# Kernel optimization log

Measured on AMD Instinct MI355X. Metric: run time of the kernel, lower is better.

The kernel has to match this reference:

```python
import jax, jax.numpy as jnp
import numpy as np

# Sizes (must match input_specs)
N_CHR, E_CHR = 50000, 500000
N_SLV, E_SLV = 30000, 300000
B = 256            # number of graphs in the batch
FEAT = 64          # num_node_feats
DIM = 128          # hidden dim
HALF = DIM // 2    # last GCN layer output
ENS = 3            # ensemble per branch type


def setup_inputs() -> dict:
    key = jax.random.key(0)
    ks = jax.random.split(key, 20)
    g = lambda k, shape, fan_in: jax.random.normal(k, shape, dtype=jnp.float32) / np.sqrt(fan_in)
    inp = {
        'chr_x': jax.random.normal(ks[0], (N_CHR, FEAT), dtype=jnp.float32),
        'slv_x': jax.random.normal(ks[1], (N_SLV, FEAT), dtype=jnp.float32),
        'chr_edge_index': jax.random.randint(ks[2], (2, E_CHR), 0, N_CHR),
        'slv_edge_index': jax.random.randint(ks[3], (2, E_SLV), 0, N_SLV),
        'chr_x_batch': jnp.sort(jax.random.randint(ks[4], (N_CHR,), 0, B)),
        'slv_x_batch': jnp.sort(jax.random.randint(ks[5], (N_SLV,), 0, B)),
        # GCN weights, stacked over ensemble (GCNConv: bias=False)
        'chr_W0': g(ks[6], (ENS, FEAT, DIM), FEAT),
        'chr_W1': g(ks[7], (ENS, DIM, DIM), DIM),
        'chr_W2': g(ks[8], (ENS, DIM, HALF), DIM),
        'slv_W0': g(ks[9], (ENS, FEAT, DIM), FEAT),
        'slv_W1': g(ks[10], (ENS, DIM, DIM), DIM),
        'slv_W2': g(ks[11], (ENS, DIM, HALF), DIM),
        # per-ensemble projection heads (nn.Linear with bias)
        'cfc_W': g(ks[12], (ENS, HALF, DIM), HALF),
        'cfc_b': jnp.zeros((ENS, DIM), dtype=jnp.float32),
        'sfc_W': g(ks[13], (ENS, HALF, DIM), HALF),
        'sfc_b': jnp.zeros((ENS, DIM), dtype=jnp.float32),
        # final MLP head
        'fc1_W': g(ks[14], (2 * ENS * DIM, DIM), 2 * ENS * DIM),
        'fc1_b': jnp.zeros((DIM,), dtype=jnp.float32),
        'fc2_W': g(ks[15], (DIM, 1), DIM),
        'fc2_b': jnp.zeros((1,), dtype=jnp.float32),
    }
    return inp


def _gcn(x, W, src, dst, n_nodes):
    # GCNConv(normalize=False, bias=False, aggr='add'):
    # out[i] = sum_{(j,i) in E} (x @ W)[j]   (no self-loops, no normalization)
    h = x @ W
    return jax.ops.segment_sum(h[src], dst, num_segments=n_nodes)


def _branch(x, W0, W1, W2, edge_index, batch_ids, n_nodes):
    src, dst = edge_index[0], edge_index[1]
    h = jax.nn.relu(_gcn(x, W0, src, dst, n_nodes))
    h = jax.nn.relu(_gcn(h, W1, src, dst, n_nodes))
    h = jax.nn.relu(_gcn(h, W2, src, dst, n_nodes))
    # global_add_pool
    return jax.ops.segment_sum(h, batch_ids, num_segments=B)  # [B, HALF]


def reference(chr_x, slv_x, chr_W0, chr_W1, chr_W2, slv_W0, slv_W1, slv_W2,
              cfc_W, cfc_b, sfc_W, sfc_b, fc1_W, fc1_b, fc2_W, fc2_b,
              chr_edge_index, slv_edge_index, chr_x_batch, slv_x_batch):
    # vmap over the ensemble dimension (independent GCN stacks share inputs)
    rep_chr = jax.vmap(lambda w0, w1, w2: _branch(chr_x, w0, w1, w2, chr_edge_index, chr_x_batch, N_CHR))(
        chr_W0, chr_W1, chr_W2)  # [ENS, B, HALF]
    rep_slv = jax.vmap(lambda w0, w1, w2: _branch(slv_x, w0, w1, w2, slv_edge_index, slv_x_batch, N_SLV))(
        slv_W0, slv_W1, slv_W2)  # [ENS, B, HALF]
    ind_chr = jax.nn.relu(jnp.einsum('ebd,edh->ebh', rep_chr, cfc_W) + cfc_b[:, None, :])  # [ENS, B, DIM]
    ind_slv = jax.nn.relu(jnp.einsum('ebd,edh->ebh', rep_slv, sfc_W) + sfc_b[:, None, :])
    # torch.cat(ind_chr + ind_slv, dim=1): chr branches first, then slv branches
    hg = jnp.concatenate([
        jnp.transpose(ind_chr, (1, 0, 2)).reshape(B, ENS * DIM),
        jnp.transpose(ind_slv, (1, 0, 2)).reshape(B, ENS * DIM)], axis=1)  # [B, 2*ENS*DIM]
    hg = jax.nn.relu(hg @ fc1_W + fc1_b)
    out = hg @ fc2_W + fc2_b  # [B, 1]
    return out
```

## Files before the change

kernel.cpp:

```cpp
#include <hip/hip_runtime.h>

#define N_CHR 50000
#define E_CHR 500000
#define N_SLV 30000
#define E_SLV 300000
#define E_TOT (E_CHR + E_SLV)
#define BATCH_B 256
#define FEAT 64
#define DIM 128
#define HALF 64
#define ENSN 3
#define CB_CHR ((N_CHR + 255) / 256)
#define CB_SLV ((N_SLV + 255) / 256)
#define CB_TOT (CB_CHR + CB_SLV)
#define NBLK 128
#define CHUNK ((E_TOT + NBLK - 1) / NBLK)

typedef unsigned int u32;
typedef unsigned short u16;
typedef __attribute__((ext_vector_type(8))) short short8;
typedef __attribute__((ext_vector_type(4))) float floatx4;
typedef __attribute__((ext_vector_type(4))) unsigned int u32x4;


__device__ inline u16 f2b(float f) {
    u32 u = __builtin_bit_cast(u32, f);
    u += 0x7FFFu + ((u >> 16) & 1u);
    return (u16)(u >> 16);
}
__device__ inline float b2f_lo(u32 v) { return __builtin_bit_cast(float, v << 16); }
__device__ inline float b2f_hi(u32 v) { return __builtin_bit_cast(float, v & 0xFFFF0000u); }
__device__ inline u32 packb(float a, float b) { return (u32)f2b(a) | ((u32)f2b(b) << 16); }

__device__ inline void acc8(float* a, u32x4 v) {
    a[0] += b2f_lo(v.x); a[1] += b2f_hi(v.x);
    a[2] += b2f_lo(v.y); a[3] += b2f_hi(v.y);
    a[4] += b2f_lo(v.z); a[5] += b2f_hi(v.z);
    a[6] += b2f_lo(v.w); a[7] += b2f_hi(v.w);
}


__global__ void xconv_k(const float* __restrict__ xc, const float* __restrict__ xs,
                        u16* __restrict__ oc, u16* __restrict__ os) {
    const int nc = N_CHR * FEAT, ns = N_SLV * FEAT;
    int i = blockIdx.x * blockDim.x + threadIdx.x;
    int stride = gridDim.x * blockDim.x;
    for (; i < nc + ns; i += stride) {
        if (i < nc) oc[i] = f2b(xc[i]);
        else os[i - nc] = f2b(xs[i - nc]);
    }
}


__global__ void wconv6_k(const float* __restrict__ cW0, const float* __restrict__ cW1,
                         const float* __restrict__ cW2, const float* __restrict__ sW0,
                         const float* __restrict__ sW1, const float* __restrict__ sW2,
                         u16* __restrict__ cW0t, u16* __restrict__ cW1t, u16* __restrict__ cW2t,
                         u16* __restrict__ sW0t, u16* __restrict__ sW1t, u16* __restrict__ sW2t) {
    int z = blockIdx.z, e = blockIdx.y;
    const float* W; u16* Wt; int K, N;
    switch (z) {
        case 0: W = cW0; Wt = cW0t; K = FEAT; N = DIM;  break;
        case 1: W = cW1; Wt = cW1t; K = DIM;  N = DIM;  break;
        case 2: W = cW2; Wt = cW2t; K = DIM;  N = HALF; break;
        case 3: W = sW0; Wt = sW0t; K = FEAT; N = DIM;  break;
        case 4: W = sW1; Wt = sW1t; K = DIM;  N = DIM;  break;
        default: W = sW2; Wt = sW2t; K = DIM; N = HALF; break;
    }
    int idx = blockIdx.x * 256 + threadIdx.x;
    if (idx >= K * N) return;
    int k = idx / N, nn = idx - k * N;
    Wt[((size_t)e * N + nn) * K + k] = f2b(W[(size_t)e * K * N + idx]);
}


__global__ __launch_bounds__(256) void hist_blocks_k(
        const int* __restrict__ cdst, const int* __restrict__ sdst,
        int* __restrict__ gh, int* __restrict__ btot) {
    __shared__ int h[CB_TOT];
    int blk = blockIdx.x, t = threadIdx.x;
    for (int i = t; i < CB_TOT; i += 256) h[i] = 0;
    __syncthreads();
    int s = blk * CHUNK, e = s + CHUNK;
    if (e > E_TOT) e = E_TOT;
    for (int i = s + t; i < e; i += 256) {
        int bkt = (i < E_CHR) ? (cdst[i] >> 8) : (CB_CHR + (sdst[i - E_CHR] >> 8));
        atomicAdd(&h[bkt], 1);
    }
    __syncthreads();
    for (int j = t; j < CB_TOT; j += 256) {
        gh[j * NBLK + blk] = h[j];
        if (h[j]) atomicAdd(&btot[j], h[j]);
    }
}

__global__ void coarse_scan_k(const int* __restrict__ cnt, int* __restrict__ off) {
    int t = threadIdx.x;
    const int PER = (CB_TOT + 63) / 64;
    int loc[PER];
    int sum = 0;
    int s = t * PER;
#pragma unroll
    for (int k = 0; k < PER; k++) {
        int i = s + k;
        int v = (i < CB_TOT) ? cnt[i] : 0;
        loc[k] = sum;
        sum += v;
    }
    int inc = sum;
#pragma unroll
    for (int o = 1; o < 64; o <<= 1) {
        int sh = __shfl_up(inc, o, 64);
        if (t >= o) inc += sh;
    }
    int pre = inc - sum;
#pragma unroll
    for (int k = 0; k < PER; k++) {
        int i = s + k;
        if (i < CB_TOT) off[i] = pre + loc[k];
    }
    if (t == 63) off[CB_TOT] = inc;
}

__global__ __launch_bounds__(NBLK) void block_base_k(int* __restrict__ gh,
                                                     const int* __restrict__ coff) {
    int j = blockIdx.x, t = threadIdx.x;
    int v = gh[j * NBLK + t];
    int lane = t & 63, wv = t >> 6;
    int inc = v;
#pragma unroll
    for (int o = 1; o < 64; o <<= 1) {
        int sh = __shfl_up(inc, o, 64);
        if (lane >= o) inc += sh;
    }
    __shared__ int ws[2];
    if (lane == 63) ws[wv] = inc;
    __syncthreads();
    int p = inc - v + (wv ? ws[0] : 0);
    gh[j * NBLK + t] = coff[j] + p;
}

__global__ __launch_bounds__(256) void scatter2_k(
        const int* __restrict__ cei, const int* __restrict__ sei,
        const int* __restrict__ gh, u32* __restrict__ staging) {
    __shared__ int cur[CB_TOT];
    int blk = blockIdx.x, t = threadIdx.x;
    for (int j = t; j < CB_TOT; j += 256) cur[j] = gh[j * NBLK + blk];
    __syncthreads();
    int s = blk * CHUNK, e = s + CHUNK;
    if (e > E_TOT) e = E_TOT;
    for (int i = s + t; i < e; i += 256) {
        int src, dst, bkt;
        if (i < E_CHR) {
            src = cei[i]; dst = cei[E_CHR + i]; bkt = dst >> 8;
        } else {
            int j2 = i - E_CHR;
            src = sei[j2]; dst = sei[E_SLV + j2]; bkt = CB_CHR + (dst >> 8);
        }
        int p = atomicAdd(&cur[bkt], 1);
        staging[p] = (u32)src | ((u32)(dst & 255) << 17);
    }
}

__device__ inline int block_exscan(int v) {
    int lane = threadIdx.x & 63, wv = threadIdx.x >> 6;
    int inc = v;
#pragma unroll
    for (int o = 1; o < 64; o <<= 1) {
        int t = __shfl_up(inc, o, 64);
        if (lane >= o) inc += t;
    }
    __shared__ int ws[4];
    if (lane == 63) ws[wv] = inc;
    __syncthreads();
    if (threadIdx.x == 0) {
        int c = 0;
#pragma unroll
        for (int k = 0; k < 4; k++) { int t = ws[k]; ws[k] = c; c += t; }
    }
    __syncthreads();
    int r = ws[wv] + inc - v;
    __syncthreads();
    return r;
}

__global__ __launch_bounds__(256) void bucket_sort_k(
        const u32* __restrict__ staging, const int* __restrict__ coff,
        int* __restrict__ off_c, int* __restrict__ off_s,
        int* __restrict__ csr_c, int* __restrict__ csr_s) {
    int b = blockIdx.x, t = threadIdx.x;
    int isS = b >= CB_CHR;
    int base = coff[b], end = coff[b + 1];
    int n = isS ? N_SLV : N_CHR;
    int* off = isS ? off_s : off_c;
    int* csr = isS ? csr_s : csr_c;
    int outBase = isS ? base - E_CHR : base;
    int nodeBase = (isS ? (b - CB_CHR) : b) << 8;
    __shared__ int hist[256];
    __shared__ int cur[256];
    hist[t] = 0;
    __syncthreads();
    for (int i = base + t; i < end; i += 256)
        atomicAdd(&hist[staging[i] >> 17], 1);
    __syncthreads();
    int p = block_exscan(hist[t]);
    int node = nodeBase + t;
    if (node <= n) off[node] = outBase + p;
    cur[t] = p;
    __syncthreads();
    for (int i = base + t; i < end; i += 256) {
        u32 v = staging[i];
        int pos = atomicAdd(&cur[v >> 17], 1);
        csr[outBase + pos] = (int)(v & 0x1FFFFu);
    }
}


__global__ __launch_bounds__(256) void agg1_k(
        const u16* __restrict__ Xc, const int* __restrict__ offc, const int* __restrict__ csrc,
        u16* __restrict__ Yc, int nc,
        const u16* __restrict__ Xs, const int* __restrict__ offs, const int* __restrict__ csrs,
        u16* __restrict__ Ys, int ns) {
    int z = blockIdx.z;
    const u32x4* X4 = (const u32x4*)(z ? Xs : Xc);
    const int* off = z ? offs : offc;
    const int* csr = z ? csrs : csrc;
    u32x4* Y4 = (u32x4*)(z ? Ys : Yc);
    int n = z ? ns : nc;
    int i = blockIdx.x * 32 + (threadIdx.x >> 3);
    if (i >= n) return;
    int l8 = threadIdx.x & 7;
    int s = off[i], e2 = off[i + 1];
    float a[8] = {0.f, 0.f, 0.f, 0.f, 0.f, 0.f, 0.f, 0.f};
    int j = s;
    for (; j + 1 < e2; j += 2) {
        u32x4 v0 = X4[(size_t)csr[j] * 8 + l8];
        u32x4 v1 = X4[(size_t)csr[j + 1] * 8 + l8];
        acc8(a, v0); acc8(a, v1);
    }
    if (j < e2) acc8(a, X4[(size_t)csr[j] * 8 + l8]);
    u32x4 o;
    o.x = packb(a[0], a[1]); o.y = packb(a[2], a[3]);
    o.z = packb(a[4], a[5]); o.w = packb(a[6], a[7]);
    Y4[(size_t)i * 8 + l8] = o;
}


__global__ __launch_bounds__(256) void aggb128_k(
        const u16* __restrict__ Hc, const int* __restrict__ offc, const int* __restrict__ csrc,
        u16* __restrict__ Yc, int nc,
        const u16* __restrict__ Hs, const int* __restrict__ offs, const int* __restrict__ csrs,
        u16* __restrict__ Ys, int ns) {
    int z = blockIdx.z, e = blockIdx.y;
    int n = z ? ns : nc;
    const int* off = z ? offs : offc;
    const int* csr = z ? csrs : csrc;
    const u32x4* He = (const u32x4*)((z ? Hs : Hc) + (size_t)e * n * DIM);
    u32x4* Ye = (u32x4*)((z ? Ys : Yc) + (size_t)e * n * DIM);
    int i = blockIdx.x * 16 + (threadIdx.x >> 4);
    if (i >= n) return;
    int l16 = threadIdx.x & 15;
    int s = off[i], e2 = off[i + 1];
    float a[8] = {0.f, 0.f, 0.f, 0.f, 0.f, 0.f, 0.f, 0.f};
    int j = s;
    for (; j + 1 < e2; j += 2) {
        u32x4 v0 = He[(size_t)csr[j] * 16 + l16];
        u32x4 v1 = He[(size_t)csr[j + 1] * 16 + l16];
        acc8(a, v0); acc8(a, v1);
    }
    if (j < e2) acc8(a, He[(size_t)csr[j] * 16 + l16]);
    u32x4 o;
    o.x = packb(a[0], a[1]); o.y = packb(a[2], a[3]);
    o.z = packb(a[4], a[5]); o.w = packb(a[6], a[7]);
    Ye[(size_t)i * 16 + l16] = o;
}


#define WPAD 8

template<int K, int COLS, bool RELU>
__global__ __launch_bounds__(256) void gemm_mfma_k(
        const u16* __restrict__ Xc, size_t esc, const u16* __restrict__ Wtc,
        u16* __restrict__ Yc, int nc,
        const u16* __restrict__ Xs, size_t ess, const u16* __restrict__ Wts,
        u16* __restrict__ Ys, int ns) {
    __shared__ u16 wlds[COLS * (K + WPAD)];
    const int z = blockIdx.z, e = blockIdx.y;
    const int n = z ? ns : nc;
    const u16* Xe = (z ? Xs : Xc) + (size_t)e * (z ? ess : esc);
    const u16* We = (z ? Wts : Wtc) + (size_t)e * COLS * K;
    u16* Ye = (z ? Ys : Yc) + (size_t)e * (size_t)n * COLS;
    for (int c = threadIdx.x; c < COLS * (K / 8); c += 256) {
        int row = c / (K / 8), seg = c - row * (K / 8);
        *(short8*)(wlds + row * (K + WPAD) + seg * 8) = *(const short8*)(We + (size_t)row * K + seg * 8);
    }
    __syncthreads();
    int wave = threadIdx.x >> 6, lane = threadIdx.x & 63;
    int quad = lane >> 4, nq = lane & 15;
    int m0 = blockIdx.x * 256 + wave * 64;
    if (m0 >= n) return;
    constexpr int NT = COLS / 16, KT = K / 32;
    floatx4 acc[4][NT];
#pragma unroll
    for (int rg = 0; rg < 4; rg++)
#pragma unroll
        for (int t = 0; t < NT; t++) acc[rg][t] = (floatx4)(0.f);
#pragma unroll
    for (int kt = 0; kt < KT; kt++) {
        int k0 = kt * 32 + quad * 8;
        short8 a[4];
#pragma unroll
        for (int rg = 0; rg < 4; rg++) {
            int row = m0 + rg * 16 + nq;
            int rc = row < n ? row : n - 1;
            a[rg] = *(const short8*)(Xe + (size_t)rc * K + k0);
        }
#pragma unroll
        for (int t = 0; t < NT; t++) {
            short8 b = *(const short8*)(wlds + (t * 16 + nq) * (K + WPAD) + k0);
#pragma unroll
            for (int rg = 0; rg < 4; rg++)
                acc[rg][t] = __builtin_amdgcn_mfma_f32_16x16x32_bf16(a[rg], b, acc[rg][t], 0, 0, 0);
        }
    }
    int rbase = quad * 4;
#pragma unroll
    for (int rg = 0; rg < 4; rg++)
#pragma unroll
        for (int t = 0; t < NT; t++)
#pragma unroll
            for (int r = 0; r < 4; r++) {
                int row = m0 + rg * 16 + rbase + r;
                if (row < n) {
                    float v = acc[rg][t][r];
                    if (RELU) v = fmaxf(v, 0.f);
                    Ye[(size_t)row * COLS + t * 16 + nq] = f2b(v);
                }
            }
}


__global__ __launch_bounds__(256) void gemm23_k(
        const u16* __restrict__ Xc, const u16* __restrict__ W1c, const u16* __restrict__ W2c,
        u16* __restrict__ Yc, int nc,
        const u16* __restrict__ Xs, const u16* __restrict__ W1s, const u16* __restrict__ W2s,
        u16* __restrict__ Ys, int ns) {
    __shared__ u16 wlds[DIM * DIM];
    __shared__ u16 hlds[4 * 32 * DIM];
    const int z = blockIdx.z, e = blockIdx.y;
    const int n = z ? ns : nc;
    const u16* Xe = (z ? Xs : Xc) + (size_t)e * (size_t)n * DIM;
    const u16* W1 = (z ? W1s : W1c) + (size_t)e * DIM * DIM;
    const u16* W2 = (z ? W2s : W2c) + (size_t)e * HALF * DIM;
    u16* Ye = (z ? Ys : Yc) + (size_t)e * (size_t)n * HALF;
    for (int c = threadIdx.x; c < DIM * (DIM / 8); c += 256) {
        int row = c >> 4, seg = c & 15;
        *(short8*)(wlds + row * DIM + ((seg ^ (row & 15)) << 3)) =
            *(const short8*)(W1 + (size_t)row * DIM + (seg << 3));
    }
    __syncthreads();
    int wave = threadIdx.x >> 6, lane = threadIdx.x & 63;
    int quad = lane >> 4, nq = lane & 15;
    int m0 = blockIdx.x * 128 + wave * 32;
    floatx4 acc[2][8];
#pragma unroll
    for (int rg = 0; rg < 2; rg++)
#pragma unroll
        for (int t = 0; t < 8; t++) acc[rg][t] = (floatx4)(0.f);
#pragma unroll
    for (int kt = 0; kt < 4; kt++) {
        int k0 = kt * 32 + quad * 8;
        short8 a[2];
#pragma unroll
        for (int rg = 0; rg < 2; rg++) {
            int row = m0 + rg * 16 + nq;
            int rc = row < n ? row : (n - 1);
            a[rg] = *(const short8*)(Xe + (size_t)rc * DIM + k0);
        }
#pragma unroll
        for (int t = 0; t < 8; t++) {
            int rb = t * 16 + nq;
            short8 b = *(const short8*)(wlds + rb * DIM + ((((kt << 2) + quad) ^ nq) << 3));
#pragma unroll
            for (int rg = 0; rg < 2; rg++)
                acc[rg][t] = __builtin_amdgcn_mfma_f32_16x16x32_bf16(a[rg], b, acc[rg][t], 0, 0, 0);
        }
    }
    u16* hw = hlds + wave * 32 * DIM;
#pragma unroll
    for (int rg = 0; rg < 2; rg++)
#pragma unroll
        for (int t = 0; t < 8; t++)
#pragma unroll
            for (int r = 0; r < 4; r++) {
                int rl = rg * 16 + quad * 4 + r;
                int col = t * 16 + nq;
                hw[rl * DIM + (((col >> 3) ^ (rl & 15)) << 3) + (col & 7)] =
                    f2b(fmaxf(acc[rg][t][r], 0.f));
            }
    __syncthreads();
    for (int c = threadIdx.x; c < HALF * (DIM / 8); c += 256) {
        int row = c >> 4, seg = c & 15;
        *(short8*)(wlds + row * DIM + ((seg ^ (row & 15)) << 3)) =
            *(const short8*)(W2 + (size_t)row * DIM + (seg << 3));
    }
    __syncthreads();
    floatx4 acc2[2][4];
#pragma unroll
    for (int rg = 0; rg < 2; rg++)
#pragma unroll
        for (int t = 0; t < 4; t++) acc2[rg][t] = (floatx4)(0.f);
#pragma unroll
    for (int kt = 0; kt < 4; kt++) {
        int k0q = (kt << 2) + quad;
        short8 a[2];
#pragma unroll
        for (int rg = 0; rg < 2; rg++) {
            int rl = rg * 16 + nq;
            a[rg] = *(const short8*)(hw + rl * DIM + ((k0q ^ (rl & 15)) << 3));
        }
#pragma unroll
        for (int t = 0; t < 4; t++) {
            int rb = t * 16 + nq;
            short8 b = *(const short8*)(wlds + rb * DIM + ((k0q ^ nq) << 3));
#pragma unroll
            for (int rg = 0; rg < 2; rg++)
                acc2[rg][t] = __builtin_amdgcn_mfma_f32_16x16x32_bf16(a[rg], b, acc2[rg][t], 0, 0, 0);
        }
    }
#pragma unroll
    for (int rg = 0; rg < 2; rg++)
#pragma unroll
        for (int t = 0; t < 4; t++)
#pragma unroll
            for (int r = 0; r < 4; r++) {
                int row = m0 + rg * 16 + quad * 4 + r;
                if (row < n) Ye[(size_t)row * HALF + t * 16 + nq] = f2b(acc2[rg][t][r]);
            }
}


__global__ __launch_bounds__(256) void agg64pool_k(
        const u16* __restrict__ Pc, const int* __restrict__ offc, const int* __restrict__ csrc,
        const int* __restrict__ batc, int nc,
        const u16* __restrict__ Ps, const int* __restrict__ offs, const int* __restrict__ csrs,
        const int* __restrict__ bats, int ns,
        float* __restrict__ rep) {
    int z = blockIdx.z, e = blockIdx.y;
    int n = z ? ns : nc;
    const int* off = z ? offs : offc;
    const int* csr = z ? csrs : csrc;
    const int* batch = z ? bats : batc;
    const u32x4* He = (const u32x4*)((z ? Ps : Pc) + (size_t)e * n * HALF);
    int i0 = blockIdx.x * 32;
    int nl = threadIdx.x >> 3, l8 = threadIdx.x & 7;
    int i = i0 + nl;
    float a[8] = {0.f, 0.f, 0.f, 0.f, 0.f, 0.f, 0.f, 0.f};
    if (i < n) {
        int s = off[i], e2 = off[i + 1];
        int j = s;
        for (; j + 1 < e2; j += 2) {
            u32x4 v0 = He[(size_t)csr[j] * 8 + l8];
            u32x4 v1 = He[(size_t)csr[j + 1] * 8 + l8];
            acc8(a, v0); acc8(a, v1);
        }
        if (j < e2) acc8(a, He[(size_t)csr[j] * 8 + l8]);
    }
    __shared__ float sm[32][64];
    __shared__ int gb[32];
#pragma unroll
    for (int k = 0; k < 8; k++) sm[nl][l8 * 8 + k] = fmaxf(a[k], 0.f);
    if (threadIdx.x < 32) gb[threadIdx.x] = (i0 + (int)threadIdx.x < n) ? batch[i0 + threadIdx.x] : -1;
    __syncthreads();
    if (threadIdx.x < 64) {
        int f = threadIdx.x;
        int colbase = z * (ENSN * HALF) + e * HALF + f;
        float acc = 0.f;
        int g = -2;
        for (int k = 0; k < 32; k++) {
            int gg = gb[k];
            if (gg != g) {
                if (g >= 0) atomicAdd(&rep[g * (2 * ENSN * HALF) + colbase], acc);
                acc = 0.f;
                g = gg;
            }
            if (gg >= 0) acc += sm[k][f];
        }
        if (g >= 0) atomicAdd(&rep[g * (2 * ENSN * HALF) + colbase], acc);
    }
}


__global__ __launch_bounds__(256) void headfinal_k(
        const float* __restrict__ rep,
        const float* __restrict__ cW, const float* __restrict__ cB,
        const float* __restrict__ sW, const float* __restrict__ sB,
        const float* __restrict__ W1, const float* __restrict__ b1,
        const float* __restrict__ W2, const float* __restrict__ b2,
        float* __restrict__ out) {
    int b = blockIdx.x, t = threadIdx.x;
    __shared__ float r[2 * ENSN * HALF];
    __shared__ float hg[2 * ENSN * DIM];
    __shared__ float red[DIM];
    for (int i = t; i < 2 * ENSN * HALF; i += 256) r[i] = rep[b * (2 * ENSN * HALF) + i];
    __syncthreads();
    for (int o = t; o < 2 * ENSN * DIM; o += 256) {
        int head = o >> 7, c = o & 127;
        int branch = head / ENSN, e = head - branch * ENSN;
        const float* W = (branch ? sW : cW) + (size_t)e * HALF * DIM;
        const float* rr = r + branch * (ENSN * HALF) + e * HALF;
        float acc = (branch ? sB : cB)[e * DIM + c];
#pragma unroll
        for (int k = 0; k < HALF; k++) acc = fmaf(rr[k], W[k * DIM + c], acc);
        hg[o] = fmaxf(acc, 0.f);
    }
    __syncthreads();
    if (t < DIM) {
        float acc = b1[t];
        for (int k = 0; k < 2 * ENSN * DIM; k++) acc = fmaf(hg[k], W1[k * DIM + t], acc);
        red[t] = fmaxf(acc, 0.f) * W2[t];
    }
    __syncthreads();
    if (t < 64) {
        float v = red[t] + red[t + 64];
#pragma unroll
        for (int o = 32; o > 0; o >>= 1) v += __shfl_down(v, o, 64);
        if (t == 0) out[b] = v + b2[0];
    }
}


extern "C" void kernel_launch(void* const* d_in, const int* in_sizes, int n_in,
                              void* d_out, int out_size, void* d_ws, size_t ws_size,
                              hipStream_t stream) {
    const float* chr_x = (const float*)d_in[0];
    const float* slv_x = (const float*)d_in[1];
    const int* chr_ei = (const int*)d_in[2];
    const int* slv_ei = (const int*)d_in[3];
    const int* chr_batch = (const int*)d_in[4];
    const int* slv_batch = (const int*)d_in[5];
    const float* chr_W0 = (const float*)d_in[6];
    const float* chr_W1 = (const float*)d_in[7];
    const float* chr_W2 = (const float*)d_in[8];
    const float* slv_W0 = (const float*)d_in[9];
    const float* slv_W1 = (const float*)d_in[10];
    const float* slv_W2 = (const float*)d_in[11];
    const float* cfc_W = (const float*)d_in[12];
    const float* cfc_b = (const float*)d_in[13];
    const float* sfc_W = (const float*)d_in[14];
    const float* sfc_b = (const float*)d_in[15];
    const float* fc1_W = (const float*)d_in[16];
    const float* fc1_b = (const float*)d_in[17];
    const float* fc2_W = (const float*)d_in[18];
    const float* fc2_b = (const float*)d_in[19];
    float* out = (float*)d_out;

    char* w = (char*)d_ws;
    auto carve = [&](size_t bytes) {
        void* p = (void*)w;
        w += (bytes + 255) & ~(size_t)255;
        return p;
    };
    int* off_chr = (int*)carve((N_CHR + 1) * sizeof(int));
    int* csr_chr = (int*)carve((size_t)E_CHR * sizeof(int));
    int* off_slv = (int*)carve((N_SLV + 1) * sizeof(int));
    int* csr_slv = (int*)carve((size_t)E_SLV * sizeof(int));
    int* btot    = (int*)carve(CB_TOT * sizeof(int));
    int* coff    = (int*)carve((CB_TOT + 1) * sizeof(int));
    int* gh      = (int*)carve((size_t)CB_TOT * NBLK * sizeof(int));
    u32* staging = (u32*)carve((size_t)E_TOT * sizeof(u32));
    u16* cW0t = (u16*)carve((size_t)ENSN * DIM * FEAT * sizeof(u16));
    u16* cW1t = (u16*)carve((size_t)ENSN * DIM * DIM * sizeof(u16));
    u16* cW2t = (u16*)carve((size_t)ENSN * HALF * DIM * sizeof(u16));
    u16* sW0t = (u16*)carve((size_t)ENSN * DIM * FEAT * sizeof(u16));
    u16* sW1t = (u16*)carve((size_t)ENSN * DIM * DIM * sizeof(u16));
    u16* sW2t = (u16*)carve((size_t)ENSN * HALF * DIM * sizeof(u16));
    u16* xb_chr = (u16*)carve((size_t)N_CHR * FEAT * sizeof(u16));
    u16* xb_slv = (u16*)carve((size_t)N_SLV * FEAT * sizeof(u16));
    float* rep = (float*)carve((size_t)BATCH_B * 2 * ENSN * HALF * sizeof(float));
    u16* aggX_c = (u16*)carve((size_t)N_CHR * FEAT * sizeof(u16));
    u16* bufP_c = (u16*)carve((size_t)ENSN * N_CHR * DIM * sizeof(u16));
    u16* bufQ_c = (u16*)carve((size_t)ENSN * N_CHR * DIM * sizeof(u16));
    u16* aggX_s = (u16*)carve((size_t)N_SLV * FEAT * sizeof(u16));
    u16* bufP_s = (u16*)carve((size_t)ENSN * N_SLV * DIM * sizeof(u16));
    u16* bufQ_s = (u16*)carve((size_t)ENSN * N_SLV * DIM * sizeof(u16));

    xconv_k<<<512, 256, 0, stream>>>(chr_x, slv_x, xb_chr, xb_slv);
    wconv6_k<<<dim3(64, ENSN, 6), 256, 0, stream>>>(chr_W0, chr_W1, chr_W2,
                                                    slv_W0, slv_W1, slv_W2,
                                                    cW0t, cW1t, cW2t, sW0t, sW1t, sW2t);

    hipMemsetAsync(btot, 0, CB_TOT * sizeof(int), stream);
    hist_blocks_k<<<NBLK, 256, 0, stream>>>(chr_ei + E_CHR, slv_ei + E_SLV, gh, btot);
    coarse_scan_k<<<1, 64, 0, stream>>>(btot, coff);
    block_base_k<<<CB_TOT, NBLK, 0, stream>>>(gh, coff);
    scatter2_k<<<NBLK, 256, 0, stream>>>(chr_ei, slv_ei, gh, staging);
    bucket_sort_k<<<CB_TOT, 256, 0, stream>>>(staging, coff, off_chr, off_slv, csr_chr, csr_slv);

    hipMemsetAsync(rep, 0, (size_t)BATCH_B * 2 * ENSN * HALF * sizeof(float), stream);

    agg1_k<<<dim3((N_CHR + 31) / 32, 1, 2), 256, 0, stream>>>(
        xb_chr, off_chr, csr_chr, aggX_c, N_CHR,
        xb_slv, off_slv, csr_slv, aggX_s, N_SLV);
    gemm_mfma_k<FEAT, DIM, true><<<dim3((N_CHR + 255) / 256, ENSN, 2), 256, 0, stream>>>(
        aggX_c, 0, cW0t, bufP_c, N_CHR, aggX_s, 0, sW0t, bufP_s, N_SLV);
    aggb128_k<<<dim3((N_CHR + 15) / 16, ENSN, 2), 256, 0, stream>>>(
        bufP_c, off_chr, csr_chr, bufQ_c, N_CHR,
        bufP_s, off_slv, csr_slv, bufQ_s, N_SLV);
    gemm23_k<<<dim3((N_CHR + 127) / 128, ENSN, 2), 256, 0, stream>>>(
        bufQ_c, cW1t, cW2t, bufP_c, N_CHR,
        bufQ_s, sW1t, sW2t, bufP_s, N_SLV);
    agg64pool_k<<<dim3((N_CHR + 31) / 32, ENSN, 2), 256, 0, stream>>>(
        bufP_c, off_chr, csr_chr, chr_batch, N_CHR,
        bufP_s, off_slv, csr_slv, slv_batch, N_SLV, rep);

    headfinal_k<<<BATCH_B, 256, 0, stream>>>(rep, cfc_W, cfc_b, sfc_W, sfc_b,
                                             fc1_W, fc1_b, fc2_W, fc2_b, out);
}
```

Baseline: 405.4 us.

## Fuse ensemble members into single aggregation pass and unroll first-layer gather

The 128-wide and 64-wide aggregation kernels now process all three ensemble members in one thread, so each CSR neighbour index and offset is loaded once instead of three times. The grid's ensemble dimension is dropped to match. The first-layer aggregation loop is unrolled by four to keep more gathers in flight. The trade-off is higher register use per thread and fewer blocks, which may reduce occupancy and latency hiding.

```diff
diff --git a/kernel.cpp b/kernel.cpp
--- a/kernel.cpp
+++ b/kernel.cpp
@@ -233,12 +233,14 @@
     int s = off[i], e2 = off[i + 1];
     float a[8] = {0.f, 0.f, 0.f, 0.f, 0.f, 0.f, 0.f, 0.f};
     int j = s;
-    for (; j + 1 < e2; j += 2) {
+    for (; j + 3 < e2; j += 4) {
         u32x4 v0 = X4[(size_t)csr[j] * 8 + l8];
         u32x4 v1 = X4[(size_t)csr[j + 1] * 8 + l8];
-        acc8(a, v0); acc8(a, v1);
-    }
-    if (j < e2) acc8(a, X4[(size_t)csr[j] * 8 + l8]);
+        u32x4 v2 = X4[(size_t)csr[j + 2] * 8 + l8];
+        u32x4 v3 = X4[(size_t)csr[j + 3] * 8 + l8];
+        acc8(a, v0); acc8(a, v1); acc8(a, v2); acc8(a, v3);
+    }
+    for (; j < e2; j++) acc8(a, X4[(size_t)csr[j] * 8 + l8]);
     u32x4 o;
     o.x = packb(a[0], a[1]); o.y = packb(a[2], a[3]);
     o.z = packb(a[4], a[5]); o.w = packb(a[6], a[7]);
@@ -246,33 +248,50 @@
 }
 
 
-__global__ __launch_bounds__(256) void aggb128_k(
+__global__ __launch_bounds__(256) void aggb128e_k(
         const u16* __restrict__ Hc, const int* __restrict__ offc, const int* __restrict__ csrc,
         u16* __restrict__ Yc, int nc,
         const u16* __restrict__ Hs, const int* __restrict__ offs, const int* __restrict__ csrs,
         u16* __restrict__ Ys, int ns) {
-    int z = blockIdx.z, e = blockIdx.y;
+    int z = blockIdx.z;
     int n = z ? ns : nc;
     const int* off = z ? offs : offc;
     const int* csr = z ? csrs : csrc;
-    const u32x4* He = (const u32x4*)((z ? Hs : Hc) + (size_t)e * n * DIM);
-    u32x4* Ye = (u32x4*)((z ? Ys : Yc) + (size_t)e * n * DIM);
+    const u16* H = z ? Hs : Hc;
+    u16* Y = z ? Ys : Yc;
+    const u32x4* H0 = (const u32x4*)H;
+    const u32x4* H1 = (const u32x4*)(H + (size_t)n * DIM);
+    const u32x4* H2 = (const u32x4*)(H + 2 * (size_t)n * DIM);
     int i = blockIdx.x * 16 + (threadIdx.x >> 4);
     if (i >= n) return;
     int l16 = threadIdx.x & 15;
     int s = off[i], e2 = off[i + 1];
-    float a[8] = {0.f, 0.f, 0.f, 0.f, 0.f, 0.f, 0.f, 0.f};
+    float a0[8] = {0,0,0,0,0,0,0,0}, a1[8] = {0,0,0,0,0,0,0,0}, a2[8] = {0,0,0,0,0,0,0,0};
     int j = s;
     for (; j + 1 < e2; j += 2) {
-        u32x4 v0 = He[(size_t)csr[j] * 16 + l16];
-        u32x4 v1 = He[(size_t)csr[j + 1] * 16 + l16];
-        acc8(a, v0); acc8(a, v1);
-    }
-    if (j < e2) acc8(a, He[(size_t)csr[j] * 16 + l16]);
+        size_t r0 = (size_t)csr[j] * 16 + l16, r1 = (size_t)csr[j + 1] * 16 + l16;
+        u32x4 p0 = H0[r0], p1 = H1[r0], p2 = H2[r0];
+        u32x4 q0 = H0[r1], q1 = H1[r1], q2 = H2[r1];
+        acc8(a0, p0); acc8(a1, p1); acc8(a2, p2);
+        acc8(a0, q0); acc8(a1, q1); acc8(a2, q2);
+    }
+    if (j < e2) {
+        size_t r0 = (size_t)csr[j] * 16 + l16;
+        acc8(a0, H0[r0]); acc8(a1, H1[r0]); acc8(a2, H2[r0]);
+    }
+    u32x4* Y0 = (u32x4*)Y;
+    u32x4* Y1 = (u32x4*)(Y + (size_t)n * DIM);
+    u32x4* Y2 = (u32x4*)(Y + 2 * (size_t)n * DIM);
     u32x4 o;
-    o.x = packb(a[0], a[1]); o.y = packb(a[2], a[3]);
-    o.z = packb(a[4], a[5]); o.w = packb(a[6], a[7]);
-    Ye[(size_t)i * 16 + l16] = o;
+    o.x = packb(a0[0], a0[1]); o.y = packb(a0[2], a0[3]);
+    o.z = packb(a0[4], a0[5]); o.w = packb(a0[6], a0[7]);
+    Y0[(size_t)i * 16 + l16] = o;
+    o.x = packb(a1[0], a1[1]); o.y = packb(a1[2], a1[3]);
+    o.z = packb(a1[4], a1[5]); o.w = packb(a1[6], a1[7]);
+    Y1[(size_t)i * 16 + l16] = o;
+    o.x = packb(a2[0], a2[1]); o.y = packb(a2[2], a2[3]);
+    o.z = packb(a2[4], a2[5]); o.w = packb(a2[6], a2[7]);
+    Y2[(size_t)i * 16 + l16] = o;
 }
 
 
@@ -440,40 +459,52 @@
 }
 
 
-__global__ __launch_bounds__(256) void agg64pool_k(
+__global__ __launch_bounds__(256) void agg64poole_k(
         const u16* __restrict__ Pc, const int* __restrict__ offc, const int* __restrict__ csrc,
         const int* __restrict__ batc, int nc,
         const u16* __restrict__ Ps, const int* __restrict__ offs, const int* __restrict__ csrs,
         const int* __restrict__ bats, int ns,
         float* __restrict__ rep) {
-    int z = blockIdx.z, e = blockIdx.y;
+    int z = blockIdx.z;
     int n = z ? ns : nc;
     const int* off = z ? offs : offc;
     const int* csr = z ? csrs : csrc;
     const int* batch = z ? bats : batc;
-    const u32x4* He = (const u32x4*)((z ? Ps : Pc) + (size_t)e * n * HALF);
+    const u16* P = z ? Ps : Pc;
+    const u32x4* P0 = (const u32x4*)P;
+    const u32x4* P1 = (const u32x4*)(P + (size_t)n * HALF);
+    const u32x4* P2 = (const u32x4*)(P + 2 * (size_t)n * HALF);
     int i0 = blockIdx.x * 32;
     int nl = threadIdx.x >> 3, l8 = threadIdx.x & 7;
     int i = i0 + nl;
-    float a[8] = {0.f, 0.f, 0.f, 0.f, 0.f, 0.f, 0.f, 0.f};
+    float a0[8] = {0,0,0,0,0,0,0,0}, a1[8] = {0,0,0,0,0,0,0,0}, a2[8] = {0,0,0,0,0,0,0,0};
     if (i < n) {
         int s = off[i], e2 = off[i + 1];
         int j = s;
         for (; j + 1 < e2; j += 2) {
-            u32x4 v0 = He[(size_t)csr[j] * 8 + l8];
-            u32x4 v1 = He[(size_t)csr[j + 1] * 8 + l8];
-            acc8(a, v0); acc8(a, v1);
-        }
-        if (j < e2) acc8(a, He[(size_t)csr[j] * 8 + l8]);
-    }
-    __shared__ float sm[32][64];
+            size_t r0 = (size_t)csr[j] * 8 + l8, r1 = (size_t)csr[j + 1] * 8 + l8;
+            u32x4 p0 = P0[r0], p1 = P1[r0], p2 = P2[r0];
+            u32x4 q0 = P0[r1], q1 = P1[r1], q2 = P2[r1];
+            acc8(a0, p0); acc8(a1, p1); acc8(a2, p2);
+            acc8(a0, q0); acc8(a1, q1); acc8(a2, q2);
+        }
+        if (j < e2) {
+            size_t r0 = (size_t)csr[j] * 8 + l8;
+            acc8(a0, P0[r0]); acc8(a1, P1[r0]); acc8(a2, P2[r0]);
+        }
+    }
+    __shared__ float sm[ENSN][32][64];
     __shared__ int gb[32];
 #pragma unroll
-    for (int k = 0; k < 8; k++) sm[nl][l8 * 8 + k] = fmaxf(a[k], 0.f);
+    for (int k = 0; k < 8; k++) {
+        sm[0][nl][l8 * 8 + k] = fmaxf(a0[k], 0.f);
+        sm[1][nl][l8 * 8 + k] = fmaxf(a1[k], 0.f);
+        sm[2][nl][l8 * 8 + k] = fmaxf(a2[k], 0.f);
+    }
     if (threadIdx.x < 32) gb[threadIdx.x] = (i0 + (int)threadIdx.x < n) ? batch[i0 + threadIdx.x] : -1;
     __syncthreads();
-    if (threadIdx.x < 64) {
-        int f = threadIdx.x;
+    if (threadIdx.x < 192) {
+        int e = threadIdx.x >> 6, f = threadIdx.x & 63;
         int colbase = z * (ENSN * HALF) + e * HALF + f;
         float acc = 0.f;
         int g = -2;
@@ -484,7 +515,7 @@
                 acc = 0.f;
                 g = gg;
             }
-            if (gg >= 0) acc += sm[k][f];
+            if (gg >= 0) acc += sm[e][k][f];
         }
         if (g >= 0) atomicAdd(&rep[g * (2 * ENSN * HALF) + colbase], acc);
     }
@@ -604,13 +635,13 @@
         xb_slv, off_slv, csr_slv, aggX_s, N_SLV);
     gemm_mfma_k<FEAT, DIM, true><<<dim3((N_CHR + 255) / 256, ENSN, 2), 256, 0, stream>>>(
         aggX_c, 0, cW0t, bufP_c, N_CHR, aggX_s, 0, sW0t, bufP_s, N_SLV);
-    aggb128_k<<<dim3((N_CHR + 15) / 16, ENSN, 2), 256, 0, stream>>>(
+    aggb128e_k<<<dim3((N_CHR + 15) / 16, 1, 2), 256, 0, stream>>>(
         bufP_c, off_chr, csr_chr, bufQ_c, N_CHR,
         bufP_s, off_slv, csr_slv, bufQ_s, N_SLV);
     gemm23_k<<<dim3((N_CHR + 127) / 128, ENSN, 2), 256, 0, stream>>>(
         bufQ_c, cW1t, cW2t, bufP_c, N_CHR,
         bufQ_s, sW1t, sW2t, bufP_s, N_SLV);
-    agg64pool_k<<<dim3((N_CHR + 31) / 32, ENSN, 2), 256, 0, stream>>>(
+    agg64poole_k<<<dim3((N_CHR + 31) / 32, 1, 2), 256, 0, stream>>>(
         bufP_c, off_chr, csr_chr, chr_batch, N_CHR,
         bufP_s, off_slv, csr_slv, slv_batch, N_SLV, rep);
 
```

New measurement: 413.3 us. Within noise of the previous version (+1.9%).
